# Performance work log

Hardware: AMD Instinct MI355X
Metric: run time of the kernel (lower is better)

The kernel has to match this reference:

```python
import math
import jax, jax.numpy as jnp
import numpy as np

NUM_HEADS = 16
LN_EPS = 1e-5


def setup_inputs() -> dict:
    key = jax.random.key(0)
    ks = jax.random.split(key, 8)
    B, S, D = 2, 1024, 1024
    L, H = 4, NUM_HEADS
    hd = D // H
    return {
        "x": jax.random.normal(ks[0], (B, S, D), jnp.float32),
        "past_k": jax.random.normal(ks[1], (L, B, H, S, hd), jnp.float32),
        "past_v": jax.random.normal(ks[2], (L, B, H, S, hd), jnp.float32),
        "past_q": jax.random.normal(ks[3], (L, B, H, S, hd), jnp.float32),
        "Wqkv": jax.random.normal(ks[4], (3 * D, D), jnp.float32) * 0.02,
        "bqkv": jnp.zeros((3 * D,), jnp.float32),
        "Wout": jax.random.normal(ks[5], (D, D), jnp.float32) * 0.02,
        "bout": jnp.zeros((D,), jnp.float32),
    }


def reference(x, past_k, past_v, past_q, Wqkv, bqkv, Wout, bout):
    B, S, D = x.shape
    H = NUM_HEADS
    hd = D // H
    scale = 1.0 / math.sqrt(hd)

    # qkv projection + head split: [B,S,D] -> [B,H,S,hd] each
    qkv = x @ Wqkv.T + bqkv  # [B,S,3D]
    q, k, v = jnp.split(qkv, 3, axis=-1)
    split = lambda t: t.reshape(B, S, H, hd).transpose(0, 2, 1, 3)
    q, k, v = split(q), split(k), split(v)

    # causal token attention scores [B,H,S,S]
    token_scores = jnp.einsum("bhqd,bhkd->bhqk", q, k) * scale
    causal = jnp.triu(jnp.ones((S, S), bool), k=1)
    token_scores = jnp.where(causal, -jnp.inf, token_scores)

    # stack past layers: [L,B,H,S,hd] -> [B,S,L,D]
    def to_full(t):
        L = t.shape[0]
        return t.transpose(1, 3, 0, 2, 4).reshape(B, S, L, D)

    mem = jnp.concatenate([to_full(past_q), to_full(past_k), to_full(past_v)], axis=2)  # [B,S,M,D], M=3L
    M = mem.shape[2]

    # layer norm (no affine) over feature dim
    mu = mem.mean(-1, keepdims=True)
    var = mem.var(-1, keepdims=True)
    mem = (mem - mu) / jnp.sqrt(var + LN_EPS)

    # reproject through K/V slices of qkv weight
    Wk, bk = Wqkv[D:2 * D], bqkv[D:2 * D]
    Wv, bv = Wqkv[2 * D:], bqkv[2 * D:]
    rk = (mem @ Wk.T + bk).reshape(B, S, M, H, hd).transpose(0, 3, 1, 2, 4)  # [B,H,S,M,hd]
    rv = (mem @ Wv.T + bv).reshape(B, S, M, H, hd).transpose(0, 3, 1, 2, 4)

    # memory scores via per-position elementwise reduce [B,H,S,M]
    mem_scores = jnp.einsum("bhsd,bhsmd->bhsm", q, rk) * scale

    scores = jnp.concatenate([token_scores, mem_scores], axis=-1)  # [B,H,S,S+M]
    weights = jax.nn.softmax(scores, axis=-1)
    token_w, mem_w = weights[..., :S], weights[..., S:]

    token_ctx = jnp.einsum("bhqk,bhkd->bhqd", token_w, v)
    mem_ctx = jnp.einsum("bhsm,bhsmd->bhsd", mem_w, rv)
    attn = token_ctx + mem_ctx  # [B,H,S,hd]

    merged = attn.transpose(0, 2, 1, 3).reshape(B, S, D)
    out = merged @ Wout.T + bout
    return out, (k, v, q)
```

## Files before the change

kernel.cpp:

```cpp
#include <hip/hip_runtime.h>

#define BATCH 2
#define SEQ   1024
#define DIM   1024
#define NH    16
#define HD    64
#define NM    12
#define NTOK  (BATCH*SEQ)
#define MEMROWS (BATCH*SEQ*NM)
#define OUTT  2097152
#define NEGBIG (-1.0e30f)

typedef __attribute__((ext_vector_type(8))) short short8;
typedef __attribute__((ext_vector_type(4))) float f32x4;

__device__ __forceinline__ float bf2f(ushort u) {
    union { unsigned int i; float f; } t; t.i = ((unsigned int)u) << 16; return t.f;
}
__device__ __forceinline__ ushort f2bf(float f) {
    union { float f; unsigned int i; } t; t.f = f;
    unsigned int i = t.i;
    unsigned int lsb = (i >> 16) & 1u;
    i += 0x7fffu + lsb;
    return (ushort)(i >> 16);
}

__global__ __launch_bounds__(256) void cvt3_kernel(
    const float* __restrict__ a, ushort* __restrict__ ab, int na4,
    const float* __restrict__ b, ushort* __restrict__ bb, int nb4,
    const float* __restrict__ c, ushort* __restrict__ cb, int nc4)
{
    int i = blockIdx.x * 256 + threadIdx.x;
    if (i >= na4 + nb4 + nc4) return;
    const float* src; ushort* dst; int j;
    if (i < na4)            { src = a; dst = ab; j = i; }
    else if (i < na4 + nb4) { src = b; dst = bb; j = i - na4; }
    else                    { src = c; dst = cb; j = i - na4 - nb4; }
    float4 v = ((const float4*)src)[j];
    ushort4 o; o.x = f2bf(v.x); o.y = f2bf(v.y); o.z = f2bf(v.z); o.w = f2bf(v.w);
    ((ushort4*)dst)[j] = o;
}


#define QKV_BLKS 384
__global__ __launch_bounds__(256) void qkv_ln_fused_kernel(
    const ushort* __restrict__ xb, const ushort* __restrict__ Wb,
    const float* __restrict__ bias, float* __restrict__ out,
    ushort* __restrict__ qkvb,
    const float* __restrict__ pq, const float* __restrict__ pk,
    const float* __restrict__ pv, ushort* __restrict__ mem_n)
{
    const int bid = blockIdx.x;
    const int tid = threadIdx.x;
    if (bid < QKV_BLKS) {
        __shared__ ushort As[128][40];
        __shared__ ushort Bs[128][40];
        const int w = tid >> 6, lane = tid & 63;
        const int n = lane & 15, qd = lane >> 4;
        const int wr = (w >> 1) * 64, wc = (w & 1) * 64;
        const int row0 = (bid / 24) * 128, col0 = (bid % 24) * 128;
        const int r1 = tid >> 2, o1 = (tid & 3) * 8;
        const int r2 = (tid + 256) >> 2, o2 = ((tid + 256) & 3) * 8;

        f32x4 acc[4][4];
#pragma unroll
        for (int mt = 0; mt < 4; mt++)
#pragma unroll
            for (int nt = 0; nt < 4; nt++) acc[mt][nt] = (f32x4){0.f, 0.f, 0.f, 0.f};

        for (int k0 = 0; k0 < 1024; k0 += 32) {
            *(short8*)&As[r1][o1] = *(const short8*)(xb + (size_t)(row0 + r1) * 1024 + k0 + o1);
            *(short8*)&As[r2][o2] = *(const short8*)(xb + (size_t)(row0 + r2) * 1024 + k0 + o2);
            *(short8*)&Bs[r1][o1] = *(const short8*)(Wb + (size_t)(col0 + r1) * 1024 + k0 + o1);
            *(short8*)&Bs[r2][o2] = *(const short8*)(Wb + (size_t)(col0 + r2) * 1024 + k0 + o2);
            __syncthreads();
            short8 af[4], bf[4];
#pragma unroll
            for (int mt = 0; mt < 4; mt++) af[mt] = *(const short8*)&As[wr + mt * 16 + n][qd * 8];
#pragma unroll
            for (int nt = 0; nt < 4; nt++) bf[nt] = *(const short8*)&Bs[wc + nt * 16 + n][qd * 8];
#pragma unroll
            for (int mt = 0; mt < 4; mt++)
#pragma unroll
                for (int nt = 0; nt < 4; nt++)
                    acc[mt][nt] = __builtin_amdgcn_mfma_f32_16x16x32_bf16(af[mt], bf[nt], acc[mt][nt], 0, 0, 0);
            __syncthreads();
        }
#pragma unroll
        for (int mt = 0; mt < 4; mt++)
#pragma unroll
            for (int nt = 0; nt < 4; nt++)
#pragma unroll
                for (int r = 0; r < 4; r++) {
                    int row = row0 + wr + mt * 16 + qd * 4 + r;
                    int col = col0 + wc + nt * 16 + n;
                    float val = acc[mt][nt][r] + bias[col];
                    int t = col >> 10, h = (col >> 6) & 15, d = col & 63;
                    int b = row >> 10, s = row & 1023;
                    size_t idx = (((size_t)(b * NH + h) * SEQ + s) * HD) + d;
                    size_t base = (t == 0) ? (size_t)3 * OUTT : (t == 1) ? (size_t)OUTT : (size_t)2 * OUTT;
                    out[base + idx] = val;
                    qkvb[(size_t)t * OUTT + idx] = f2bf(val);
                }
    } else {
        const int wid = tid >> 6, lane = tid & 63;
        const int r = (bid - QKV_BLKS) * 4 + wid;
        const int idx = r % NM;
        const int bs = r / NM;
        const int s = bs & (SEQ - 1);
        const int b = bs >> 10;
        const int c = idx >> 2;
        const int l = idx & 3;
        const float* src = (c == 0) ? pq : ((c == 1) ? pk : pv);
        const size_t base = ((size_t)(l * BATCH + b) * NH) * (SEQ * HD) + (size_t)s * HD;

        float4 v4[4];
        float sum = 0.f, sumsq = 0.f;
#pragma unroll
        for (int p = 0; p < 4; p++) {
            int h = p * 4 + (lane >> 4);
            int d = (lane & 15) * 4;
            float4 v = *(const float4*)(src + base + (size_t)h * (SEQ * HD) + d);
            v4[p] = v;
            sum   += v.x + v.y + v.z + v.w;
            sumsq += v.x * v.x + v.y * v.y + v.z * v.z + v.w * v.w;
        }
#pragma unroll
        for (int off = 32; off > 0; off >>= 1) {
            sum   += __shfl_xor(sum, off);
            sumsq += __shfl_xor(sumsq, off);
        }
        float mu  = sum * (1.f / 1024.f);
        float var = fmaxf(sumsq * (1.f / 1024.f) - mu * mu, 0.f);
        float inv = rsqrtf(var + 1e-5f);
        ushort* dst = mem_n + (size_t)r * 1024;
#pragma unroll
        for (int p = 0; p < 4; p++) {
            int dp = (p * 64 + lane) * 4;
            ushort4 o;
            o.x = f2bf((v4[p].x - mu) * inv);
            o.y = f2bf((v4[p].y - mu) * inv);
            o.z = f2bf((v4[p].z - mu) * inv);
            o.w = f2bf((v4[p].w - mu) * inv);
            *(ushort4*)(dst + dp) = o;
        }
    }
}

__global__ __launch_bounds__(256) void mfma_out_kernel(
    const ushort* __restrict__ Ab, const ushort* __restrict__ Wb,
    const float* __restrict__ bias, float* __restrict__ C)
{
    __shared__ ushort As[128][40];
    __shared__ ushort Bs[128][40];
    const int tid = threadIdx.x;
    const int w = tid >> 6, lane = tid & 63;
    const int n = lane & 15, qd = lane >> 4;
    const int wr = (w >> 1) * 64, wc = (w & 1) * 64;
    const int row0 = blockIdx.y * 128, col0 = blockIdx.x * 128;
    const int r1 = tid >> 2, o1 = (tid & 3) * 8;
    const int r2 = (tid + 256) >> 2, o2 = ((tid + 256) & 3) * 8;

    f32x4 acc[4][4];
#pragma unroll
    for (int mt = 0; mt < 4; mt++)
#pragma unroll
        for (int nt = 0; nt < 4; nt++) acc[mt][nt] = (f32x4){0.f, 0.f, 0.f, 0.f};

    for (int k0 = 0; k0 < 1024; k0 += 32) {
        *(short8*)&As[r1][o1] = *(const short8*)(Ab + (size_t)(row0 + r1) * 1024 + k0 + o1);
        *(short8*)&As[r2][o2] = *(const short8*)(Ab + (size_t)(row0 + r2) * 1024 + k0 + o2);
        *(short8*)&Bs[r1][o1] = *(const short8*)(Wb + (size_t)(col0 + r1) * 1024 + k0 + o1);
        *(short8*)&Bs[r2][o2] = *(const short8*)(Wb + (size_t)(col0 + r2) * 1024 + k0 + o2);
        __syncthreads();
        short8 af[4], bf[4];
#pragma unroll
        for (int mt = 0; mt < 4; mt++) af[mt] = *(const short8*)&As[wr + mt * 16 + n][qd * 8];
#pragma unroll
        for (int nt = 0; nt < 4; nt++) bf[nt] = *(const short8*)&Bs[wc + nt * 16 + n][qd * 8];
#pragma unroll
        for (int mt = 0; mt < 4; mt++)
#pragma unroll
            for (int nt = 0; nt < 4; nt++)
                acc[mt][nt] = __builtin_amdgcn_mfma_f32_16x16x32_bf16(af[mt], bf[nt], acc[mt][nt], 0, 0, 0);
        __syncthreads();
    }
#pragma unroll
    for (int mt = 0; mt < 4; mt++)
#pragma unroll
        for (int nt = 0; nt < 4; nt++)
#pragma unroll
            for (int r = 0; r < 4; r++) {
                int row = row0 + wr + mt * 16 + qd * 4 + r;
                int col = col0 + wc + nt * 16 + n;
                C[(size_t)row * 1024 + col] = acc[mt][nt][r] + bias[col];
            }
}

__global__ __launch_bounds__(256) void mfma_qproj_kernel(
    const ushort* __restrict__ qkvb, const ushort* __restrict__ Wkb,
    ushort* __restrict__ qproj)
{
    __shared__ ushort As[128][40];
    __shared__ ushort Bs[128][40];
    const int tid = threadIdx.x;
    const int w = tid >> 6, lane = tid & 63;
    const int n = lane & 15, qd = lane >> 4;
    const int wr = (w >> 1) * 64, wc = (w & 1) * 64;
    const int row0 = blockIdx.y * 128, col0 = blockIdx.x * 128;
    const int h = blockIdx.z;
    const int b = row0 >> 10, s0 = row0 & 1023;
    const ushort* Abase = qkvb + ((size_t)(b * NH + h) * SEQ + s0) * HD;
    const int r1 = tid >> 2, o1 = (tid & 3) * 8;
    const int r2 = (tid + 256) >> 2, o2 = ((tid + 256) & 3) * 8;
    const int bkk = tid >> 3, bc0 = (tid & 7) * 16;

    f32x4 acc[4][4];
#pragma unroll
    for (int mt = 0; mt < 4; mt++)
#pragma unroll
        for (int nt = 0; nt < 4; nt++) acc[mt][nt] = (f32x4){0.f, 0.f, 0.f, 0.f};

    for (int k0 = 0; k0 < 64; k0 += 32) {
        *(short8*)&As[r1][o1] = *(const short8*)(Abase + (size_t)r1 * HD + k0 + o1);
        *(short8*)&As[r2][o2] = *(const short8*)(Abase + (size_t)r2 * HD + k0 + o2);
        {
            const ushort* bsrc = Wkb + (size_t)(h * HD + k0 + bkk) * 1024 + col0 + bc0;
            ushort tmp[16];
            *(short8*)&tmp[0] = *(const short8*)bsrc;
            *(short8*)&tmp[8] = *(const short8*)(bsrc + 8);
#pragma unroll
            for (int i = 0; i < 16; i++) Bs[bc0 + i][bkk] = tmp[i];
        }
        __syncthreads();
        short8 af[4], bf[4];
#pragma unroll
        for (int mt = 0; mt < 4; mt++) af[mt] = *(const short8*)&As[wr + mt * 16 + n][qd * 8];
#pragma unroll
        for (int nt = 0; nt < 4; nt++) bf[nt] = *(const short8*)&Bs[wc + nt * 16 + n][qd * 8];
#pragma unroll
        for (int mt = 0; mt < 4; mt++)
#pragma unroll
            for (int nt = 0; nt < 4; nt++)
                acc[mt][nt] = __builtin_amdgcn_mfma_f32_16x16x32_bf16(af[mt], bf[nt], acc[mt][nt], 0, 0, 0);
        __syncthreads();
    }
#pragma unroll
    for (int mt = 0; mt < 4; mt++)
#pragma unroll
        for (int nt = 0; nt < 4; nt++)
#pragma unroll
            for (int r = 0; r < 4; r++) {
                int token = row0 + wr + mt * 16 + qd * 4 + r;
                int col = col0 + wc + nt * 16 + n;
                qproj[((size_t)token * NH + h) * 1024 + col] = f2bf(acc[mt][nt][r]);
            }
}

__global__ __launch_bounds__(256) void mfma_vproj_kernel(
    const ushort* __restrict__ wvecb, const ushort* __restrict__ Wvb,
    const float* __restrict__ bv, const float* __restrict__ wmem,
    ushort* __restrict__ mergedb)
{
    __shared__ ushort As[128][40];
    __shared__ ushort Bs[64][40];
    const int tid = threadIdx.x;
    const int w = tid >> 6, lane = tid & 63;
    const int n = lane & 15, qd = lane >> 4;
    const int wr = (w >> 1) * 64, wc = (w & 1) * 32;
    const int row0 = blockIdx.x * 128;
    const int h = blockIdx.y;
    const int r1 = tid >> 2, o1 = (tid & 3) * 8;
    const int r2 = (tid + 256) >> 2, o2 = ((tid + 256) & 3) * 8;

    f32x4 acc[4][2];
#pragma unroll
    for (int mt = 0; mt < 4; mt++)
#pragma unroll
        for (int nt = 0; nt < 2; nt++) acc[mt][nt] = (f32x4){0.f, 0.f, 0.f, 0.f};

    for (int k0 = 0; k0 < 1024; k0 += 32) {
        *(short8*)&As[r1][o1] = *(const short8*)(wvecb + ((size_t)(row0 + r1) * NH + h) * 1024 + k0 + o1);
        *(short8*)&As[r2][o2] = *(const short8*)(wvecb + ((size_t)(row0 + r2) * NH + h) * 1024 + k0 + o2);
        *(short8*)&Bs[r1 & 63][o1] = *(const short8*)(Wvb + (size_t)(h * HD + (r1 & 63)) * 1024 + k0 + o1);
        __syncthreads();
        short8 af[4], bf[2];
#pragma unroll
        for (int mt = 0; mt < 4; mt++) af[mt] = *(const short8*)&As[wr + mt * 16 + n][qd * 8];
#pragma unroll
        for (int nt = 0; nt < 2; nt++) bf[nt] = *(const short8*)&Bs[wc + nt * 16 + n][qd * 8];
#pragma unroll
        for (int mt = 0; mt < 4; mt++)
#pragma unroll
            for (int nt = 0; nt < 2; nt++)
                acc[mt][nt] = __builtin_amdgcn_mfma_f32_16x16x32_bf16(af[mt], bf[nt], acc[mt][nt], 0, 0, 0);
        __syncthreads();
    }
#pragma unroll
    for (int mt = 0; mt < 4; mt++)
#pragma unroll
        for (int nt = 0; nt < 2; nt++)
#pragma unroll
            for (int r = 0; r < 4; r++) {
                int token = row0 + wr + mt * 16 + qd * 4 + r;
                int d = wc + nt * 16 + n;
                float ws = wmem[((size_t)token * NH + h) * 16 + 12];
                size_t mi = (size_t)token * DIM + h * HD + d;
                float val = bf2f(mergedb[mi]) + acc[mt][nt][r] + ws * bv[h * HD + d];
                mergedb[mi] = f2bf(val);
            }
}

__global__ __launch_bounds__(256) void msc_fused_kernel(
    const ushort* __restrict__ qproj, const ushort* __restrict__ mem_n,
    const ushort* __restrict__ qkvb, const float* __restrict__ bqkv,
    float* __restrict__ msc)
{
    const int tid = threadIdx.x;
    const int w = tid >> 6, lane = tid & 63;
    const int n = lane & 15, qd = lane >> 4;
    const int bs = blockIdx.x * 4 + w;

    float qbk = 0.f;
    if (lane < 16) {
        int b = bs >> 10, s = bs & 1023;
        const ushort* qrow = qkvb + ((size_t)(b * NH + lane) * SEQ + s) * HD;
        const float* bk = bqkv + DIM + lane * HD;
#pragma unroll
        for (int d = 0; d < HD; d++) qbk += bf2f(qrow[d]) * bk[d];
    }
    f32x4 acc = (f32x4){0.f, 0.f, 0.f, 0.f};
    const ushort* qpB = qproj + ((size_t)bs * NH + n) * 1024;
    const int mrow = (n < NM) ? n : 0;
    const ushort* mmB = mem_n + ((size_t)bs * NM + mrow) * 1024;
    for (int k0 = 0; k0 < 1024; k0 += 32) {
        short8 af = *(const short8*)(qpB + k0 + qd * 8);
        short8 bf = *(const short8*)(mmB + k0 + qd * 8);
        acc = __builtin_amdgcn_mfma_f32_16x16x32_bf16(af, bf, acc, 0, 0, 0);
    }
#pragma unroll
    for (int r = 0; r < 4; r++) {
        int h = qd * 4 + r;
        float qb = __shfl(qbk, h);
        if (n < NM)
            msc[((size_t)bs * NH + h) * NM + n] = 0.125f * (acc[r] + qb);
    }
}

#define TQ 64
#define TK 64
__global__ __launch_bounds__(512) void flash_attn_kernel(
    const ushort* __restrict__ qkvb, const float* __restrict__ msc,
    ushort* __restrict__ mergedb, float* __restrict__ wmem)
{
    __shared__ __align__(16) char smem[55296];
    ushort (*Ks)[TK][72]  = (ushort (*)[TK][72])smem;
    ushort (*Vt)[HD][72]  = (ushort (*)[HD][72])(smem + 18432);
    ushort (*Ps)[16][72]  = (ushort (*)[16][72])(smem + 36864);
    float  (*cbuf)[64][25] = (float (*)[64][25])smem;

    const int bxr = blockIdx.x;
    const int qt = (bxr & 1) ? (bxr >> 1) : (15 - (bxr >> 1));
    const int bh = blockIdx.y;
    const int b = bh >> 4, h = bh & 15;
    const int tid = threadIdx.x;
    const int w = tid >> 6;
    const int g = w >> 2;
    const int wq = w & 3;
    const int lane = tid & 63;
    const int n = lane & 15;
    const int qd = lane >> 4;

    const ushort* qb = qkvb;
    const ushort* kb = qkvb + (size_t)OUTT;
    const ushort* vb = qkvb + (size_t)2 * OUTT;
    const size_t headoff = (size_t)bh * SEQ * HD;

    const int qrow0 = qt * TQ + wq * 16;
    const ushort* qp = qb + headoff + (size_t)(qrow0 + n) * HD;
    short8 qf0 = *(const short8*)(qp + qd * 8);
    short8 qf1 = *(const short8*)(qp + 32 + qd * 8);

    float mrow[4], lrow[4];
    f32x4 Oacc[4];
#pragma unroll
    for (int r = 0; r < 4; r++) { mrow[r] = NEGBIG; lrow[r] = 0.f; }
#pragma unroll
    for (int nt = 0; nt < 4; nt++) Oacc[nt] = (f32x4){0.f, 0.f, 0.f, 0.f};

    const int gtid = tid & 255;
    const int key = gtid >> 2;
    const int c0 = (gtid & 3) * 16;
    const int nsteps = (qt + 2) >> 1;

    for (int step = 0; step < nsteps; ++step) {
        const int kt = 2 * step + g;
        const bool act = (kt <= qt);
        if (act) {
            const ushort* kg = kb + headoff + (size_t)(kt * TK + key) * HD + c0;
            *(short8*)&Ks[g][key][c0]     = *(const short8*)kg;
            *(short8*)&Ks[g][key][c0 + 8] = *(const short8*)(kg + 8);
            const ushort* vg = vb + headoff + (size_t)(kt * TK + key) * HD + c0;
            ushort vs[16];
            *(short8*)&vs[0] = *(const short8*)vg;
            *(short8*)&vs[8] = *(const short8*)(vg + 8);
#pragma unroll
            for (int i = 0; i < 16; i++) Vt[g][c0 + i][key] = vs[i];
        }
        __syncthreads();
        if (act) {
            f32x4 sacc[4];
#pragma unroll
            for (int kc = 0; kc < 4; kc++) {
                short8 kf0 = *(const short8*)&Ks[g][kc * 16 + n][qd * 8];
                short8 kf1 = *(const short8*)&Ks[g][kc * 16 + n][32 + qd * 8];
                f32x4 z = (f32x4){0.f, 0.f, 0.f, 0.f};
                z = __builtin_amdgcn_mfma_f32_16x16x32_bf16(qf0, kf0, z, 0, 0, 0);
                z = __builtin_amdgcn_mfma_f32_16x16x32_bf16(qf1, kf1, z, 0, 0, 0);
                sacc[kc] = z;
            }
            const bool diag = (kt == qt);
#pragma unroll
            for (int kc = 0; kc < 4; kc++) {
#pragma unroll
                for (int r = 0; r < 4; r++) {
                    float sv = sacc[kc][r] * 0.125f;
                    if (diag) {
                        int qrow = qrow0 + qd * 4 + r;
                        int kk = kt * TK + kc * 16 + n;
                        if (kk > qrow) sv = NEGBIG;
                    }
                    sacc[kc][r] = sv;
                }
            }
            float alpha[4];
#pragma unroll
            for (int r = 0; r < 4; r++) {
                float mx = fmaxf(fmaxf(sacc[0][r], sacc[1][r]), fmaxf(sacc[2][r], sacc[3][r]));
                mx = fmaxf(mx, __shfl_xor(mx, 1));
                mx = fmaxf(mx, __shfl_xor(mx, 2));
                mx = fmaxf(mx, __shfl_xor(mx, 4));
                mx = fmaxf(mx, __shfl_xor(mx, 8));
                float mnew = fmaxf(mrow[r], mx);
                alpha[r] = __expf(mrow[r] - mnew);
                mrow[r] = mnew;
            }
            float psum[4] = {0.f, 0.f, 0.f, 0.f};
#pragma unroll
            for (int kc = 0; kc < 4; kc++) {
#pragma unroll
                for (int r = 0; r < 4; r++) {
                    float p = __expf(sacc[kc][r] - mrow[r]);
                    psum[r] += p;
                    Ps[w][qd * 4 + r][kc * 16 + n] = f2bf(p);
                }
            }
#pragma unroll
            for (int r = 0; r < 4; r++) {
                float ps = psum[r];
                ps += __shfl_xor(ps, 1);
                ps += __shfl_xor(ps, 2);
                ps += __shfl_xor(ps, 4);
                ps += __shfl_xor(ps, 8);
                lrow[r] = alpha[r] * lrow[r] + ps;
            }
#pragma unroll
            for (int nt = 0; nt < 4; nt++)
#pragma unroll
                for (int r = 0; r < 4; r++)
                    Oacc[nt][r] *= alpha[r];
            short8 pf0 = *(const short8*)&Ps[w][n][qd * 8];
            short8 pf1 = *(const short8*)&Ps[w][n][32 + qd * 8];
#pragma unroll
            for (int nt = 0; nt < 4; nt++) {
                short8 vf0 = *(const short8*)&Vt[g][nt * 16 + n][qd * 8];
                short8 vf1 = *(const short8*)&Vt[g][nt * 16 + n][32 + qd * 8];
                f32x4 z = Oacc[nt];
                z = __builtin_amdgcn_mfma_f32_16x16x32_bf16(pf0, vf0, z, 0, 0, 0);
                z = __builtin_amdgcn_mfma_f32_16x16x32_bf16(pf1, vf1, z, 0, 0, 0);
                Oacc[nt] = z;
            }
        }
        __syncthreads();
    }

    if (g == 1) {
        float* cb = cbuf[wq][lane];
#pragma unroll
        for (int nt = 0; nt < 4; nt++)
#pragma unroll
            for (int r = 0; r < 4; r++) cb[nt * 4 + r] = Oacc[nt][r];
#pragma unroll
        for (int r = 0; r < 4; r++) { cb[16 + r] = mrow[r]; cb[20 + r] = lrow[r]; }
    }
    __syncthreads();
    if (g == 1) return;

    {
        const float* cb = cbuf[wq][lane];
#pragma unroll
        for (int r = 0; r < 4; r++) {
            float m1 = cb[16 + r], l1 = cb[20 + r];
            float mnew = fmaxf(mrow[r], m1);
            float a0 = __expf(mrow[r] - mnew);
            float a1 = __expf(m1 - mnew);
            lrow[r] = a0 * lrow[r] + a1 * l1;
#pragma unroll
            for (int nt = 0; nt < 4; nt++)
                Oacc[nt][r] = a0 * Oacc[nt][r] + a1 * cb[nt * 4 + r];
            mrow[r] = mnew;
        }
    }

#pragma unroll
    for (int r = 0; r < 4; r++) {
        int srow = qrow0 + qd * 4 + r;
        const float* mp = msc + ((size_t)(b * SEQ + srow) * NH + h) * NM;
        float mm = NEGBIG;
#pragma unroll
        for (int j = 0; j < NM; j++) mm = fmaxf(mm, mp[j]);
        float mf = fmaxf(mrow[r], mm);
        float al = __expf(mrow[r] - mf);
        float msum = 0.f;
#pragma unroll
        for (int j = 0; j < NM; j++) msum += __expf(mp[j] - mf);
        float lf = al * lrow[r] + msum;
        float inv = 1.f / lf;
        float scale = al * inv;
        ushort* mrow_out = mergedb + (size_t)(b * SEQ + srow) * DIM + h * HD;
#pragma unroll
        for (int nt = 0; nt < 4; nt++)
            mrow_out[nt * 16 + n] = f2bf(Oacc[nt][r] * scale);
        size_t wb = ((size_t)(b * SEQ + srow) * NH + h) * 16;
        if (n < 12)       wmem[wb + n]  = __expf(mp[n] - mf) * inv;
        else if (n == 12) wmem[wb + 12] = msum * inv;
    }
}

__global__ __launch_bounds__(256) void wvec_kernel(
    const float* __restrict__ wmem, const ushort* __restrict__ mem_n,
    ushort* __restrict__ wvecb)
{
    __shared__ ushort memL[NM][1032];
    __shared__ float wL[NH][NM];
    const int bs = blockIdx.x;
    const int tid = threadIdx.x;

    for (int t = tid; t < NM * 256; t += 256) {
        int m = t >> 8, c4 = (t & 255) << 2;
        *(ushort4*)&memL[m][c4] = *(const ushort4*)(mem_n + ((size_t)bs * NM + m) * 1024 + c4);
    }
    if (tid < NH * NM) {
        int h = tid / NM, m = tid % NM;
        wL[h][m] = wmem[((size_t)bs * NH + h) * 16 + m];
    }
    __syncthreads();

    for (int h = 0; h < NH; h++) {
#pragma unroll
        for (int c0 = 0; c0 < 1024; c0 += 256) {
            int c = c0 + tid;
            float acc = 0.f;
#pragma unroll
            for (int m = 0; m < NM; m++)
                acc = fmaf(wL[h][m], bf2f(memL[m][c]), acc);
            wvecb[((size_t)bs * NH + h) * 1024 + c] = f2bf(acc);
        }
    }
}

extern "C" void kernel_launch(void* const* d_in, const int* in_sizes, int n_in,
                              void* d_out, int out_size, void* d_ws, size_t ws_size,
                              hipStream_t stream) {
    const float* x    = (const float*)d_in[0];
    const float* pk   = (const float*)d_in[1];
    const float* pv   = (const float*)d_in[2];
    const float* pq   = (const float*)d_in[3];
    const float* Wqkv = (const float*)d_in[4];
    const float* bqkv = (const float*)d_in[5];
    const float* Wout = (const float*)d_in[6];
    const float* bout = (const float*)d_in[7];
    float* out = (float*)d_out;

    ushort* mem_n  = (ushort*)d_ws;
    ushort* qproj  = mem_n + (size_t)MEMROWS * 1024;
    ushort* wvecb  = qproj;
    float*  msc    = (float*)(qproj + (size_t)NTOK * NH * 1024);
    float*  wmem   = msc + (size_t)NTOK * NH * NM;
    ushort* qkvb   = (ushort*)(wmem + (size_t)NTOK * NH * 16);
    ushort* Wqkvb  = qkvb + (size_t)3 * OUTT;
    ushort* Woutb  = Wqkvb + (size_t)3072 * 1024;
    ushort* xb     = Woutb + (size_t)1024 * 1024;
    ushort* mergedb = xb;

    const int na4 = NTOK * DIM / 4, nb4 = 3 * DIM * DIM / 4, nc4 = DIM * DIM / 4;

    cvt3_kernel<<<(na4 + nb4 + nc4 + 255) / 256, 256, 0, stream>>>(
        x, xb, na4, Wqkv, Wqkvb, nb4, Wout, Woutb, nc4);
    qkv_ln_fused_kernel<<<QKV_BLKS + MEMROWS / 4, 256, 0, stream>>>(
        xb, Wqkvb, bqkv, out, qkvb, pq, pk, pv, mem_n);
    mfma_qproj_kernel<<<dim3(8, 16, NH), 256, 0, stream>>>(
        qkvb, Wqkvb + (size_t)DIM * DIM, qproj);
    msc_fused_kernel<<<NTOK / 4, 256, 0, stream>>>(qproj, mem_n, qkvb, bqkv, msc);
    flash_attn_kernel<<<dim3(16, 32), 512, 0, stream>>>(qkvb, msc, mergedb, wmem);
    wvec_kernel<<<NTOK, 256, 0, stream>>>(wmem, mem_n, wvecb);
    mfma_vproj_kernel<<<dim3(16, NH), 256, 0, stream>>>(
        wvecb, Wqkvb + (size_t)2 * DIM * DIM, bqkv + 2 * DIM, wmem, mergedb);
    mfma_out_kernel<<<dim3(8, 16), 256, 0, stream>>>(mergedb, Woutb, bout, out);
}
```

Measured before the change: 360.4 us.

## Fuse q-projection through Wk into memory-score kernel, dropping qproj buffer

Replaces the separate q·Wk projection kernel, which wrote a large bf16 intermediate (NTOK*NH*1024), and the msc kernel that read it back. The new kernel computes the projected queries in 64-column chunks in shared memory and immediately contracts them against the normalized memory rows. This removes the round trip of a ~64MB intermediate through global memory and one launch. In exchange, each block reloads and transposes Wk chunks for only 8 tokens, which adds redundant weight traffic and LDS transposes, and uses smaller MFMA tiles.

```diff
diff --git a/kernel.cpp b/kernel.cpp
--- a/kernel.cpp
+++ b/kernel.cpp
@@ -197,66 +197,6 @@
             }
 }
 
-__global__ __launch_bounds__(256) void mfma_qproj_kernel(
-    const ushort* __restrict__ qkvb, const ushort* __restrict__ Wkb,
-    ushort* __restrict__ qproj)
-{
-    __shared__ ushort As[128][40];
-    __shared__ ushort Bs[128][40];
-    const int tid = threadIdx.x;
-    const int w = tid >> 6, lane = tid & 63;
-    const int n = lane & 15, qd = lane >> 4;
-    const int wr = (w >> 1) * 64, wc = (w & 1) * 64;
-    const int row0 = blockIdx.y * 128, col0 = blockIdx.x * 128;
-    const int h = blockIdx.z;
-    const int b = row0 >> 10, s0 = row0 & 1023;
-    const ushort* Abase = qkvb + ((size_t)(b * NH + h) * SEQ + s0) * HD;
-    const int r1 = tid >> 2, o1 = (tid & 3) * 8;
-    const int r2 = (tid + 256) >> 2, o2 = ((tid + 256) & 3) * 8;
-    const int bkk = tid >> 3, bc0 = (tid & 7) * 16;
-
-    f32x4 acc[4][4];
-#pragma unroll
-    for (int mt = 0; mt < 4; mt++)
-#pragma unroll
-        for (int nt = 0; nt < 4; nt++) acc[mt][nt] = (f32x4){0.f, 0.f, 0.f, 0.f};
-
-    for (int k0 = 0; k0 < 64; k0 += 32) {
-        *(short8*)&As[r1][o1] = *(const short8*)(Abase + (size_t)r1 * HD + k0 + o1);
-        *(short8*)&As[r2][o2] = *(const short8*)(Abase + (size_t)r2 * HD + k0 + o2);
-        {
-            const ushort* bsrc = Wkb + (size_t)(h * HD + k0 + bkk) * 1024 + col0 + bc0;
-            ushort tmp[16];
-            *(short8*)&tmp[0] = *(const short8*)bsrc;
-            *(short8*)&tmp[8] = *(const short8*)(bsrc + 8);
-#pragma unroll
-            for (int i = 0; i < 16; i++) Bs[bc0 + i][bkk] = tmp[i];
-        }
-        __syncthreads();
-        short8 af[4], bf[4];
-#pragma unroll
-        for (int mt = 0; mt < 4; mt++) af[mt] = *(const short8*)&As[wr + mt * 16 + n][qd * 8];
-#pragma unroll
-        for (int nt = 0; nt < 4; nt++) bf[nt] = *(const short8*)&Bs[wc + nt * 16 + n][qd * 8];
-#pragma unroll
-        for (int mt = 0; mt < 4; mt++)
-#pragma unroll
-            for (int nt = 0; nt < 4; nt++)
-                acc[mt][nt] = __builtin_amdgcn_mfma_f32_16x16x32_bf16(af[mt], bf[nt], acc[mt][nt], 0, 0, 0);
-        __syncthreads();
-    }
-#pragma unroll
-    for (int mt = 0; mt < 4; mt++)
-#pragma unroll
-        for (int nt = 0; nt < 4; nt++)
-#pragma unroll
-            for (int r = 0; r < 4; r++) {
-                int token = row0 + wr + mt * 16 + qd * 4 + r;
-                int col = col0 + wc + nt * 16 + n;
-                qproj[((size_t)token * NH + h) * 1024 + col] = f2bf(acc[mt][nt][r]);
-            }
-}
-
 __global__ __launch_bounds__(256) void mfma_vproj_kernel(
     const ushort* __restrict__ wvecb, const ushort* __restrict__ Wvb,
     const float* __restrict__ bv, const float* __restrict__ wmem,
@@ -311,39 +251,110 @@
             }
 }
 
-__global__ __launch_bounds__(256) void msc_fused_kernel(
-    const ushort* __restrict__ qproj, const ushort* __restrict__ mem_n,
-    const ushort* __restrict__ qkvb, const float* __restrict__ bqkv,
+#define MSC_T 8
+__global__ __launch_bounds__(256) void msc_direct_kernel(
+    const ushort* __restrict__ qkvb, const ushort* __restrict__ mem_n,
+    const ushort* __restrict__ Wkb, const float* __restrict__ bqkv,
     float* __restrict__ msc)
 {
+    __shared__ ushort qs[MSC_T][16][72];
+    __shared__ ushort memc[MSC_T][12][72];
+    __shared__ ushort qpc[MSC_T][16][72];
+    __shared__ ushort wks[4][64][72];
+    __shared__ float  qbkL[MSC_T][16];
+
     const int tid = threadIdx.x;
     const int w = tid >> 6, lane = tid & 63;
     const int n = lane & 15, qd = lane >> 4;
-    const int bs = blockIdx.x * 4 + w;
-
-    float qbk = 0.f;
-    if (lane < 16) {
-        int b = bs >> 10, s = bs & 1023;
-        const ushort* qrow = qkvb + ((size_t)(b * NH + lane) * SEQ + s) * HD;
-        const float* bk = bqkv + DIM + lane * HD;
-#pragma unroll
-        for (int d = 0; d < HD; d++) qbk += bf2f(qrow[d]) * bk[d];
-    }
-    f32x4 acc = (f32x4){0.f, 0.f, 0.f, 0.f};
-    const ushort* qpB = qproj + ((size_t)bs * NH + n) * 1024;
-    const int mrow = (n < NM) ? n : 0;
-    const ushort* mmB = mem_n + ((size_t)bs * NM + mrow) * 1024;
-    for (int k0 = 0; k0 < 1024; k0 += 32) {
-        short8 af = *(const short8*)(qpB + k0 + qd * 8);
-        short8 bf = *(const short8*)(mmB + k0 + qd * 8);
-        acc = __builtin_amdgcn_mfma_f32_16x16x32_bf16(af, bf, acc, 0, 0, 0);
-    }
-#pragma unroll
-    for (int r = 0; r < 4; r++) {
-        int h = qd * 4 + r;
-        float qb = __shfl(qbk, h);
-        if (n < NM)
-            msc[((size_t)bs * NH + h) * NM + n] = 0.125f * (acc[r] + qb);
+    const int t0 = blockIdx.x * MSC_T;
+
+    {
+        const int rid = tid >> 1, half = tid & 1;
+        const int t = rid >> 4, h = rid & 15;
+        const int g = t0 + t, b = g >> 10, s = g & 1023;
+        const ushort* src = qkvb + (((size_t)(b * NH + h) * SEQ + s) * HD) + half * 32;
+        *(short8*)&qs[t][h][half * 32]      = *(const short8*)(src);
+        *(short8*)&qs[t][h][half * 32 + 8]  = *(const short8*)(src + 8);
+        *(short8*)&qs[t][h][half * 32 + 16] = *(const short8*)(src + 16);
+        *(short8*)&qs[t][h][half * 32 + 24] = *(const short8*)(src + 24);
+    }
+    __syncthreads();
+    if (tid < 128) {
+        const int t = tid >> 4, h = tid & 15;
+        const float* bk = bqkv + DIM + h * HD;
+        float s = 0.f;
+#pragma unroll
+        for (int d = 0; d < HD; d++) s += bf2f(qs[t][h][d]) * bk[d];
+        qbkL[t][h] = s;
+    }
+
+    f32x4 acc[2];
+    acc[0] = (f32x4){0.f, 0.f, 0.f, 0.f};
+    acc[1] = (f32x4){0.f, 0.f, 0.f, 0.f};
+
+    for (int ch = 0; ch < 16; ch++) {
+        const int c0 = ch * 64;
+        __syncthreads();
+#pragma unroll
+        for (int i = 0; i < 3; i++) {
+            int sid = i * 256 + tid;
+            int row = sid >> 3, o8 = (sid & 7) * 8;
+            int t = row / 12, m = row % 12;
+            *(short8*)&memc[t][m][o8] =
+                *(const short8*)(mem_n + ((size_t)(t0 + t) * NM + m) * 1024 + c0 + o8);
+        }
+#pragma unroll
+        for (int hh = 0; hh < 4; hh++) {
+            const int h = w * 4 + hh;
+            const ushort* wsrc = Wkb + (size_t)(h * HD + lane) * 1024 + c0;
+#pragma unroll
+            for (int j = 0; j < 4; j++) {
+                ushort t16[16];
+                *(short8*)&t16[0] = *(const short8*)(wsrc + j * 16);
+                *(short8*)&t16[8] = *(const short8*)(wsrc + j * 16 + 8);
+#pragma unroll
+                for (int c = 0; c < 16; c++) wks[w][j * 16 + c][lane] = t16[c];
+            }
+            short8 af0 = *(const short8*)&qs[n & 7][h][qd * 8];
+            short8 af1 = *(const short8*)&qs[n & 7][h][32 + qd * 8];
+#pragma unroll
+            for (int nt = 0; nt < 4; nt++) {
+                short8 bf0 = *(const short8*)&wks[w][nt * 16 + n][qd * 8];
+                short8 bf1 = *(const short8*)&wks[w][nt * 16 + n][32 + qd * 8];
+                f32x4 z = (f32x4){0.f, 0.f, 0.f, 0.f};
+                z = __builtin_amdgcn_mfma_f32_16x16x32_bf16(af0, bf0, z, 0, 0, 0);
+                z = __builtin_amdgcn_mfma_f32_16x16x32_bf16(af1, bf1, z, 0, 0, 0);
+                if (qd < 2) {
+#pragma unroll
+                    for (int r = 0; r < 4; r++)
+                        qpc[qd * 4 + r][h][nt * 16 + n] = f2bf(z[r]);
+                }
+            }
+        }
+        __syncthreads();
+#pragma unroll
+        for (int p = 0; p < 2; p++) {
+            const int tw = w + p * 4;
+            const int mrow = (n < NM) ? n : 0;
+            short8 af0 = *(const short8*)&qpc[tw][n][qd * 8];
+            short8 af1 = *(const short8*)&qpc[tw][n][32 + qd * 8];
+            short8 bf0 = *(const short8*)&memc[tw][mrow][qd * 8];
+            short8 bf1 = *(const short8*)&memc[tw][mrow][32 + qd * 8];
+            acc[p] = __builtin_amdgcn_mfma_f32_16x16x32_bf16(af0, bf0, acc[p], 0, 0, 0);
+            acc[p] = __builtin_amdgcn_mfma_f32_16x16x32_bf16(af1, bf1, acc[p], 0, 0, 0);
+        }
+    }
+    if (n < NM) {
+#pragma unroll
+        for (int p = 0; p < 2; p++) {
+            const int tw = w + p * 4;
+            const size_t gt = t0 + tw;
+#pragma unroll
+            for (int r = 0; r < 4; r++) {
+                int h = qd * 4 + r;
+                msc[(gt * NH + h) * NM + n] = 0.125f * (acc[p][r] + qbkL[tw][h]);
+            }
+        }
     }
 }
 
@@ -583,9 +594,8 @@
     float* out = (float*)d_out;
 
     ushort* mem_n  = (ushort*)d_ws;
-    ushort* qproj  = mem_n + (size_t)MEMROWS * 1024;
-    ushort* wvecb  = qproj;
-    float*  msc    = (float*)(qproj + (size_t)NTOK * NH * 1024);
+    ushort* wvecb  = mem_n + (size_t)MEMROWS * 1024;
+    float*  msc    = (float*)(wvecb + (size_t)NTOK * NH * 1024);
     float*  wmem   = msc + (size_t)NTOK * NH * NM;
     ushort* qkvb   = (ushort*)(wmem + (size_t)NTOK * NH * 16);
     ushort* Wqkvb  = qkvb + (size_t)3 * OUTT;
@@ -599,9 +609,8 @@
         x, xb, na4, Wqkv, Wqkvb, nb4, Wout, Woutb, nc4);
     qkv_ln_fused_kernel<<<QKV_BLKS + MEMROWS / 4, 256, 0, stream>>>(
         xb, Wqkvb, bqkv, out, qkvb, pq, pk, pv, mem_n);
-    mfma_qproj_kernel<<<dim3(8, 16, NH), 256, 0, stream>>>(
-        qkvb, Wqkvb + (size_t)DIM * DIM, qproj);
-    msc_fused_kernel<<<NTOK / 4, 256, 0, stream>>>(qproj, mem_n, qkvb, bqkv, msc);
+    msc_direct_kernel<<<NTOK / MSC_T, 256, 0, stream>>>(
+        qkvb, mem_n, Wqkvb + (size_t)DIM * DIM, bqkv, msc);
     flash_attn_kernel<<<dim3(16, 32), 512, 0, stream>>>(qkvb, msc, mergedb, wmem);
     wvec_kernel<<<NTOK, 256, 0, stream>>>(wmem, mem_n, wvecb);
     mfma_vproj_kernel<<<dim3(16, NH), 256, 0, stream>>>(
```

Result: slower. 398.6 us (+10.6%).
